# Kernel tuning notes

Measured on AMD Instinct MI355X. Metric: run time of the kernel, lower is better.

Reference implementation:

```python
import jax, jax.numpy as jnp
import numpy as np

C = 16      # internal_channel
G = 8       # deform groups
KK = 9      # 3x3 kernel taps


def conv2d(x, w, b, pad):
    y = jax.lax.conv_general_dilated(
        x, w, window_strides=(1, 1), padding=[(pad, pad), (pad, pad)],
        dimension_numbers=('NCHW', 'OIHW', 'NCHW'))
    return y + b[None, :, None, None]


def feature_extraction(img, p):
    f1 = jax.nn.relu(conv2d(img, p['conv1_w'], p['conv1_b'], 1))   # [B,C,H,W]
    f2 = jax.nn.relu(conv2d(f1, p['conv2_w'], p['conv2_b'], 0))    # [B,C,H-2,W-2]
    f3 = jax.nn.relu(conv2d(f2, p['conv3_w'], p['conv3_b'], 0))    # [B,C,H-4,W-4]
    return [f1, f2, f3]


def deform_conv2d(x, offset, w, b, groups):
    # torchvision deform_conv2d semantics: stride 1, pad 1, dilation 1, 3x3,
    # zero out-of-bounds bilinear sampling, explicit offsets.
    B, Ci, H, W = x.shape
    Cg = Ci // groups
    off = offset.reshape(B, groups, KK, 2, H, W)
    oy, ox = off[:, :, :, 0], off[:, :, :, 1]          # [B,G,K,H,W]
    k = jnp.arange(KK)
    ky = (k // 3).reshape(1, 1, KK, 1, 1).astype(x.dtype)
    kx = (k % 3).reshape(1, 1, KK, 1, 1).astype(x.dtype)
    hh = jnp.arange(H, dtype=x.dtype).reshape(1, 1, 1, H, 1)
    ww = jnp.arange(W, dtype=x.dtype).reshape(1, 1, 1, 1, W)
    ys = hh - 1.0 + ky + oy                            # sample rows
    xs = ww - 1.0 + kx + ox                            # sample cols
    y0 = jnp.floor(ys); x0 = jnp.floor(xs)
    dy = ys - y0; dx = xs - x0
    y0i = y0.astype(jnp.int32); x0i = x0.astype(jnp.int32)
    xg = x.reshape(B, groups, Cg, H * W)

    def gather(iy, ix):
        valid = ((iy >= 0) & (iy < H) & (ix >= 0) & (ix < W)).astype(x.dtype)
        idx = jnp.clip(iy, 0, H - 1) * W + jnp.clip(ix, 0, W - 1)
        g = jnp.take_along_axis(xg, idx.reshape(B, groups, 1, KK * H * W), axis=3)
        return g.reshape(B, groups, Cg, KK, H, W) * valid[:, :, None]

    v = (gather(y0i, x0i) * ((1 - dy) * (1 - dx))[:, :, None]
         + gather(y0i, x0i + 1) * ((1 - dy) * dx)[:, :, None]
         + gather(y0i + 1, x0i) * (dy * (1 - dx))[:, :, None]
         + gather(y0i + 1, x0i + 1) * (dy * dx)[:, :, None])
    v = v.reshape(B, Ci, KK, H, W)
    out = jnp.einsum('ocK,bcKhw->bohw', w.reshape(w.shape[0], Ci, KK), v)
    return out + b[None, :, None, None]


def setup_inputs() -> dict:
    key = jax.random.key(0)
    ks = jax.random.split(key, 12)
    B, H, Wd = 4, 256, 256
    d = {
        'ref_image': jax.random.normal(ks[0], (B, 3, H, Wd), jnp.float32),
        'unreg_image': jax.random.normal(ks[1], (B, 3, H, Wd), jnp.float32),
        'conv1_w': jax.random.normal(ks[2], (C, 3, 3, 3), jnp.float32) * 0.05,
        'conv1_b': jnp.zeros((C,), jnp.float32),
        'conv2_w': jax.random.normal(ks[3], (C, C, 3, 3), jnp.float32) * 0.05,
        'conv2_b': jnp.zeros((C,), jnp.float32),
        'conv3_w': jax.random.normal(ks[4], (C, C, 3, 3), jnp.float32) * 0.05,
        'conv3_b': jnp.zeros((C,), jnp.float32),
        'off1_w': jax.random.normal(ks[5], (2 * G * KK, 2 * C, 3, 3), jnp.float32) * 0.01,
        'off1_b': jnp.zeros((2 * G * KK,), jnp.float32),
        'off2_w': jax.random.normal(ks[6], (2 * G * KK, 2 * C, 3, 3), jnp.float32) * 0.01,
        'off2_b': jnp.zeros((2 * G * KK,), jnp.float32),
        'off3_w': jax.random.normal(ks[7], (2 * G * KK, 2 * C, 3, 3), jnp.float32) * 0.01,
        'off3_b': jnp.zeros((2 * G * KK,), jnp.float32),
        'dcn_w': jax.random.normal(ks[8], (C, C, 3, 3), jnp.float32) * 0.05,
        'dcn_b': jnp.zeros((C,), jnp.float32),
    }
    return d


def reference(ref_image, unreg_image, conv1_w, conv1_b, conv2_w, conv2_b,
              conv3_w, conv3_b, off1_w, off1_b, off2_w, off2_b,
              off3_w, off3_b, dcn_w, dcn_b):
    p = dict(conv1_w=conv1_w, conv1_b=conv1_b, conv2_w=conv2_w, conv2_b=conv2_b,
             conv3_w=conv3_w, conv3_b=conv3_b)
    ref_f = feature_extraction(ref_image, p)
    unr_f = feature_extraction(unreg_image, p)
    off_ws = [(off1_w, off1_b), (off2_w, off2_b), (off3_w, off3_b)]
    aligned = []
    for i in range(3):
        cat = jnp.concatenate([ref_f[i], unr_f[i]], axis=1)          # [B,2C,Hi,Wi]
        offset = jax.nn.relu(conv2d(cat, off_ws[i][0], off_ws[i][1], 1))
        aligned.append(deform_conv2d(unr_f[i], offset, dcn_w, dcn_b, G))
    return tuple(aligned)
```

## Files before the change

kernel.cpp:

```cpp
#include <hip/hip_runtime.h>


typedef __attribute__((ext_vector_type(8))) short bf16x8;
typedef __attribute__((ext_vector_type(4))) float f32x4;
typedef __attribute__((ext_vector_type(2))) float f32x2;

__device__ inline unsigned short f2bf(float f) {
    union { float f; unsigned int u; } x; x.f = f;
    unsigned int u = x.u;
    u += 0x7fffu + ((u >> 16) & 1u);
    return (unsigned short)(u >> 16);
}
__device__ inline float bf2f(unsigned short u) {
    union { unsigned int i; float f; } x; x.i = ((unsigned int)u) << 16;
    return x.f;
}
__device__ inline f32x2 ld2(const float* p) {
    f32x2 v;
    __builtin_memcpy(&v, p, 8);
    return v;
}

__device__ inline void xcd_swz(int& bx, int& by, int& bz) {
    const int gx = gridDim.x, gy = gridDim.y, gz = gridDim.z;
    const int hw = blockIdx.x + gx * (blockIdx.y + gy * blockIdx.z);
    const int per = (gx * gy * gz) >> 3;
    const int lg = (hw & 7) * per + (hw >> 3);
    bz = lg / (gx * gy);
    const int rem = lg - bz * gx * gy;
    by = rem / gx;
    bx = rem - by * gx;
}

__global__ __launch_bounds__(256) void conv1_kernel(
    const float* __restrict__ ref, const float* __restrict__ unr,
    const float* __restrict__ w, const float* __restrict__ bias,
    unsigned short* __restrict__ outA, unsigned short* __restrict__ outB,
    float* __restrict__ pU)
{
    const int H = 256, W = 256;
    __shared__ float sIn[3][18][18];
    const int tx = threadIdx.x, ty = threadIdx.y;
    const int tid = ty * 16 + tx;
    const int bx = blockIdx.x, by = blockIdx.y, bz8 = blockIdx.z;
    const int isUnr = bz8 >> 2, bb = bz8 & 3;
    const float* in = isUnr ? unr : ref;
    unsigned short* outCL = isUnr ? outB : outA;
    const int x0 = bx * 16 - 1, y0 = by * 16 - 1;

    for (int idx = tid; idx < 3 * 324; idx += 256) {
        int c = idx / 324, rem = idx % 324, r = rem / 18, col = rem % 18;
        int gy = y0 + r, gx = x0 + col;
        float v = 0.f;
        if (gy >= 0 && gy < H && gx >= 0 && gx < W)
            v = in[((bb * 3 + c) * H + gy) * W + gx];
        sIn[c][r][col] = v;
    }
    __syncthreads();

    const int y = by * 16 + ty, x = bx * 16 + tx;
    float acc[16];
#pragma unroll
    for (int o = 0; o < 16; o++) acc[o] = bias[o];
#pragma unroll
    for (int ci = 0; ci < 3; ci++) {
        float xv[9];
#pragma unroll
        for (int r = 0; r < 3; r++)
#pragma unroll
            for (int c = 0; c < 3; c++)
                xv[r * 3 + c] = sIn[ci][ty + r][tx + c];
#pragma unroll
        for (int o = 0; o < 16; o++) {
            const float* wp = w + (o * 3 + ci) * 9;
#pragma unroll
            for (int u = 0; u < 9; u++) acc[o] += wp[u] * xv[u];
        }
    }
#pragma unroll
    for (int o = 0; o < 16; o++) acc[o] = fmaxf(acc[o], 0.f);

    const size_t HW = (size_t)H * W;
    unsigned short tmp[16];
#pragma unroll
    for (int o = 0; o < 16; o++) tmp[o] = f2bf(acc[o]);
    unsigned short* op = outCL + ((size_t)bb * HW + (size_t)y * W + x) * 16;
    *(bf16x8*)(op) = *(bf16x8*)&tmp[0];
    *(bf16x8*)(op + 8) = *(bf16x8*)&tmp[8];
    if (isUnr) {
#pragma unroll
        for (int o = 0; o < 16; o++)
            pU[((size_t)(bb * 16 + o) * H + y) * W + x] = acc[o];
    }
}

__global__ __launch_bounds__(512, 4) void c16m_kernel(
    const unsigned short* __restrict__ inA, const unsigned short* __restrict__ inB,
    const unsigned short* __restrict__ Bc16, const float* __restrict__ bias,
    unsigned short* __restrict__ outA, unsigned short* __restrict__ outB,
    float* __restrict__ pU, int Hout, int Wout)
{
    const int Hin = Hout + 2, Win = Wout + 2;
    __shared__ __align__(16) unsigned short sC[324 * 16];
    __shared__ float sT[16][16][17];
    const int tid = threadIdx.x;
    const int bx = blockIdx.x, by = blockIdx.y, bz8 = blockIdx.z;
    const int isUnr = bz8 >> 2, bz = bz8 & 3;
    const unsigned short* inCL = isUnr ? inB : inA;
    unsigned short* outCL = isUnr ? outB : outA;
    const int x0 = bx * 16, y0 = by * 16;

    for (int idx = tid; idx < 648; idx += 512) {
        int px = idx >> 1, half = idx & 1;
        int r = px / 18, c = px % 18;
        int gy = min(y0 + r, Hin - 1), gx = min(x0 + c, Win - 1);
        const bf16x8* p = (const bf16x8*)(inCL +
            (((size_t)bz * Hin * Win + (size_t)gy * Win + gx) * 16 + 8 * half));
        *(bf16x8*)&sC[px * 16 + 8 * half] = *p;
    }
    __syncthreads();

    const int w = tid >> 6, l = tid & 63;
    const int q = l >> 4, j16 = l & 15;
    const float bv = bias[j16];
    f32x4 acc0 = {bv, bv, bv, bv}, acc1 = {bv, bv, bv, bv};

#pragma unroll
    for (int t = 0; t < 5; ++t) {
        const int u = (t == 4) ? 8 : 2 * t + (q >> 1);
        const int dr = u / 3, dc = u % 3;
        bf16x8 a0 = *(const bf16x8*)&sC[(((w) + dr) * 18 + (j16 + dc)) * 16 + (q & 1) * 8];
        bf16x8 a1 = *(const bf16x8*)&sC[(((w + 8) + dr) * 18 + (j16 + dc)) * 16 + (q & 1) * 8];
        bf16x8 b = *(const bf16x8*)&Bc16[(t * 64 + l) * 8];
        acc0 = __builtin_amdgcn_mfma_f32_16x16x32_bf16(a0, b, acc0, 0, 0, 0);
        acc1 = __builtin_amdgcn_mfma_f32_16x16x32_bf16(a1, b, acc1, 0, 0, 0);
    }
#pragma unroll
    for (int r = 0; r < 4; ++r) { acc0[r] = fmaxf(acc0[r], 0.f); acc1[r] = fmaxf(acc1[r], 0.f); }

    const int yA = y0 + w, yB = y0 + w + 8;
    const size_t HWo = (size_t)Hout * Wout;
#pragma unroll
    for (int r = 0; r < 4; ++r) {
        int x = x0 + 4 * q + r;
        if (yA < Hout && x < Wout)
            outCL[((size_t)bz * HWo + (size_t)yA * Wout + x) * 16 + j16] = f2bf(acc0[r]);
        if (yB < Hout && x < Wout)
            outCL[((size_t)bz * HWo + (size_t)yB * Wout + x) * 16 + j16] = f2bf(acc1[r]);
    }

    if (isUnr) {
#pragma unroll
        for (int r = 0; r < 4; ++r) {
            sT[w][j16][4 * q + r] = acc0[r];
            sT[w + 8][j16][4 * q + r] = acc1[r];
        }
        __syncthreads();
        const int ch = tid >> 5, yy = (tid >> 1) & 15, half = tid & 1;
        const int yo = y0 + yy;
        if (yo < Hout) {
            float* dst = pU + ((size_t)(bz * 16 + ch) * Hout + yo) * Wout + x0 + half * 8;
#pragma unroll
            for (int i = 0; i < 8; ++i) {
                int x = x0 + half * 8 + i;
                if (x < Wout) dst[i] = sT[yy][ch][half * 8 + i];
            }
        }
    }
}

__global__ __launch_bounds__(512) void prep_kernel(
    const float* __restrict__ o1w, const float* __restrict__ o2w, const float* __restrict__ o3w,
    const float* __restrict__ o1b, const float* __restrict__ o2b, const float* __restrict__ o3b,
    const float* __restrict__ dw, const float* __restrict__ c2w, const float* __restrict__ c3w,
    unsigned short* __restrict__ Bfrag, float* __restrict__ biasPrep, float* __restrict__ dwT,
    unsigned short* __restrict__ Bc16)
{
    const int lvl = blockIdx.y;
    const float* Wt = (lvl == 0) ? o1w : (lvl == 1) ? o2w : o3w;
    const float* Bb = (lvl == 0) ? o1b : (lvl == 1) ? o2b : o3b;
    int idx = blockIdx.x * 512 + threadIdx.x;
    int j = idx & 7;
    int l = (idx >> 3) & 63;
    int tu = idx >> 9;
    int t = tu / 9, u = tu % 9;
    int q = l >> 4, n16 = l & 15;
    int ci = 8 * q + j;
    int g = n16 >> 1, d = n16 & 1;
    int ch = g * 18 + t * 2 + d;
    Bfrag[lvl * 41472 + idx] = f2bf(Wt[(ch * 32 + ci) * 9 + u]);
    if (blockIdx.x == 0 && threadIdx.x < 144) {
        int n = threadIdx.x;
        int tt = n >> 4, nn = n & 15;
        biasPrep[lvl * 144 + n] = Bb[(nn >> 1) * 18 + tt * 2 + (nn & 1)];
    }
    if (lvl == 0 && blockIdx.x == 1) {
        for (int i = threadIdx.x; i < 2304; i += 512) {
            int c = i / 144, rem = i % 144, k = rem / 16, o = rem & 15;
            dwT[i] = dw[(o * 16 + c) * 9 + k];
        }
    }
    if (lvl == 2 && blockIdx.x >= 20 && blockIdx.x < 30) {
        int i2 = (blockIdx.x - 20) * 512 + threadIdx.x;
        int cw = i2 / 2560, rem = i2 % 2560;
        int jj = rem & 7, ll = (rem >> 3) & 63, tt = rem >> 9;
        int qq = ll >> 4, oo = ll & 15;
        int uu = (tt == 4) ? 8 : 2 * tt + (qq >> 1);
        int cc = (qq & 1) * 8 + jj;
        const float* wsel = cw ? c3w : c2w;
        float val = (tt == 4 && qq >= 2) ? 0.f : wsel[(oo * 16 + cc) * 9 + uu];
        Bc16[i2] = f2bf(val);
    }
}

#define CP 40
__global__ __launch_bounds__(512, 4) void offconv_kernel(
    const unsigned short* __restrict__ refCL, const unsigned short* __restrict__ unrCL,
    const unsigned short* __restrict__ Bfrag, const float* __restrict__ biasPrep,
    unsigned short* __restrict__ offbuf, int bbBase, int BN, int H, int W)
{
    __shared__ __align__(16) unsigned short sIn[18 * 18 * CP];
    __shared__ __align__(16) unsigned short sB[2][4608];
    const int tid = threadIdx.x;
    int bx, by, bz;
    xcd_swz(bx, by, bz);
    const int bb = bbBase + bz;
    const int x0 = bx * 16 - 1, y0 = by * 16 - 1;
    const size_t HW = (size_t)H * W;

    auto loadB = [&](int t, int buf) {
        const bf16x8* src = (const bf16x8*)(Bfrag + (size_t)t * 4608);
        bf16x8* dst = (bf16x8*)&sB[buf][0];
        dst[tid] = src[tid];
        if (tid < 64) dst[512 + tid] = src[512 + tid];
    };
    loadB(0, 0);

    for (int idx = tid; idx < 1296; idx += 512) {
        int px = idx >> 2, ch8 = idx & 3;
        int r = px / 18, c = px % 18;
        int gy = y0 + r, gx = x0 + c;
        bf16x8 v = {};
        if (gy >= 0 && gy < H && gx >= 0 && gx < W) {
            const unsigned short* src = (ch8 < 2) ? refCL : unrCL;
            v = *(const bf16x8*)(src + (((size_t)bb * HW + (size_t)gy * W + gx) * 16 + (ch8 & 1) * 8));
        }
        *(bf16x8*)&sIn[px * CP + ch8 * 8] = v;
    }
    __syncthreads();

    const int w = tid >> 6, l = tid & 63;
    const int q = l >> 4, j16 = l & 15;

    bf16x8 a0[9], a1[9];
#pragma unroll
    for (int u = 0; u < 9; ++u) {
        int dr = u / 3, dc = u % 3;
        a0[u] = *(const bf16x8*)&sIn[((w + dr) * 18 + (j16 + dc)) * CP + 8 * q];
        a1[u] = *(const bf16x8*)&sIn[((w + 8 + dr) * 18 + (j16 + dc)) * CP + 8 * q];
    }
    const int yA = by * 16 + w, yB = by * 16 + w + 8;

    float bvv[9];
#pragma unroll
    for (int t = 0; t < 9; ++t) bvv[t] = biasPrep[t * 16 + j16];

#pragma unroll 1
    for (int t = 0; t < 9; ++t) {
        if (t < 8) loadB(t + 1, (t + 1) & 1);
        const unsigned short* bp = &sB[t & 1][0];
        const float bv = bvv[t];
        f32x4 acc0 = {bv, bv, bv, bv}, acc1 = {bv, bv, bv, bv};
#pragma unroll
        for (int u = 0; u < 9; ++u) {
            bf16x8 b = *(const bf16x8*)&bp[(u * 64 + l) * 8];
            acc0 = __builtin_amdgcn_mfma_f32_16x16x32_bf16(a0[u], b, acc0, 0, 0, 0);
            acc1 = __builtin_amdgcn_mfma_f32_16x16x32_bf16(a1[u], b, acc1, 0, 0, 0);
        }
        const size_t tb = ((size_t)t * BN + bz) * HW;
#pragma unroll
        for (int r = 0; r < 4; ++r) {
            int x = bx * 16 + 4 * q + r;
            if (yA < H && x < W)
                offbuf[(tb + (size_t)yA * W + x) * 16 + j16] = f2bf(fmaxf(acc0[r], 0.f));
            if (yB < H && x < W)
                offbuf[(tb + (size_t)yB * W + x) * 16 + j16] = f2bf(fmaxf(acc1[r], 0.f));
        }
        __syncthreads();
    }
}

__global__ __launch_bounds__(256) void deform_kernel(
    const float* __restrict__ unrP, const unsigned short* __restrict__ offbuf,
    const float* __restrict__ dwT, const float* __restrict__ dcn_b,
    float* __restrict__ out, int bbBase, int BN, int H, int W)
{
    const int tx = threadIdx.x & 15, ty = threadIdx.x >> 4;
    int bxs, bys, bz;
    xcd_swz(bxs, bys, bz);
    const int bb = bbBase + bz;
    const int xr = bxs * 16 + tx, yr = bys * 16 + ty;
    const int x = min(xr, W - 1), y = min(yr, H - 1);
    const size_t HW = (size_t)H * W;
    const float* base = unrP + (size_t)bb * 16 * HW;
    const size_t pxi = (size_t)y * W + x;

    f32x4 pv[4];
#pragma unroll
    for (int i = 0; i < 4; ++i)
        pv[i] = (f32x4){dcn_b[4 * i], dcn_b[4 * i + 1], dcn_b[4 * i + 2], dcn_b[4 * i + 3]};

#pragma unroll 1
    for (int k = 0; k < 9; ++k) {
        const unsigned short* po = offbuf + (((size_t)k * BN + bz) * HW + pxi) * 16;
        bf16x8 s0 = *(const bf16x8*)(po);
        bf16x8 s1 = *(const bf16x8*)(po + 8);
        float ov[16];
#pragma unroll
        for (int i = 0; i < 8; ++i) ov[i] = bf2f((unsigned short)s0[i]);
#pragma unroll
        for (int i = 0; i < 8; ++i) ov[8 + i] = bf2f((unsigned short)s1[i]);

        const float fy = (float)(y - 1 + k / 3);
        const float fx = (float)(x - 1 + k % 3);
#pragma unroll
        for (int g = 0; g < 8; ++g) {
            float oy = ov[2 * g], ox = ov[2 * g + 1];
            float ys = fy + oy, xs = fx + ox;
            float y0f = floorf(ys), x0f = floorf(xs);
            float dy = ys - y0f, dx = xs - x0f;
            int iy0 = (int)y0f, ix0 = (int)x0f;
            int iy1 = iy0 + 1, ix1 = ix0 + 1;
            float vy0 = (iy0 >= 0 && iy0 < H) ? 1.f : 0.f;
            float vy1 = (iy1 >= 0 && iy1 < H) ? 1.f : 0.f;
            float vx0 = (ix0 >= 0 && ix0 < W) ? 1.f : 0.f;
            float vx1 = (ix1 < W) ? 1.f : 0.f;
            int pb = min(max(ix0, 0), W - 2);
            const bool swp = (ix0 != pb);
            float wx0 = (1.f - dx) * vx0, wx1 = dx * vx1;
            float wA = swp ? wx1 : wx0;
            float wB = swp ? wx0 : wx1;
            float wy0 = (1.f - dy) * vy0, wy1 = dy * vy1;
            int cy0 = min(max(iy0, 0), H - 1), cy1 = min(max(iy1, 0), H - 1);
            const float* p0 = base + (size_t)(2 * g) * HW;
            const float* p1 = base + (size_t)(2 * g + 1) * HW;
            const int ib0 = cy0 * W + pb, ib1 = cy1 * W + pb;
            f32x2 a0 = ld2(p0 + ib0), a1 = ld2(p0 + ib1);
            f32x2 b0 = ld2(p1 + ib0), b1 = ld2(p1 + ib1);
            float wA0 = wy0 * wA, wB0 = wy0 * wB, wA1 = wy1 * wA, wB1 = wy1 * wB;
            float v0 = wA0 * a0.x + wB0 * a0.y + wA1 * a1.x + wB1 * a1.y;
            float v1 = wA0 * b0.x + wB0 * b0.y + wA1 * b1.x + wB1 * b1.y;
            const f32x4* wv0 = (const f32x4*)(dwT + ((2 * g) * 9 + k) * 16);
            const f32x4* wv1 = (const f32x4*)(dwT + ((2 * g + 1) * 9 + k) * 16);
#pragma unroll
            for (int i = 0; i < 4; ++i) pv[i] += v0 * wv0[i];
#pragma unroll
            for (int i = 0; i < 4; ++i) pv[i] += v1 * wv1[i];
        }
    }

    if (xr < W && yr < H) {
#pragma unroll
        for (int i = 0; i < 4; ++i)
#pragma unroll
            for (int c = 0; c < 4; ++c)
                out[((size_t)(bb * 16 + 4 * i + c) * H + y) * W + x] = pv[i][c];
    }
}

extern "C" void kernel_launch(void* const* d_in, const int* in_sizes, int n_in,
                              void* d_out, int out_size, void* d_ws, size_t ws_size,
                              hipStream_t stream) {
    (void)in_sizes; (void)n_in; (void)out_size;
    const float* ref = (const float*)d_in[0];
    const float* unr = (const float*)d_in[1];
    const float* c1w = (const float*)d_in[2];  const float* c1b = (const float*)d_in[3];
    const float* c2w = (const float*)d_in[4];  const float* c2b = (const float*)d_in[5];
    const float* c3w = (const float*)d_in[6];  const float* c3b = (const float*)d_in[7];
    const float* o1w = (const float*)d_in[8];  const float* o1b = (const float*)d_in[9];
    const float* o2w = (const float*)d_in[10]; const float* o2b = (const float*)d_in[11];
    const float* o3w = (const float*)d_in[12]; const float* o3b = (const float*)d_in[13];
    const float* dw  = (const float*)d_in[14]; const float* db  = (const float*)d_in[15];

    float* out0 = (float*)d_out;
    float* out1 = out0 + (size_t)4 * 16 * 256 * 256;
    float* out2 = out1 + (size_t)4 * 16 * 254 * 254;

    unsigned short* fA = (unsigned short*)d_ws;
    unsigned short* fB = fA + (size_t)4 * 65536 * 16;
    unsigned short* fC = fB + (size_t)4 * 65536 * 16;
    unsigned short* fD = fC + (size_t)4 * 64516 * 16;
    float* pU = (float*)(fD + (size_t)4 * 64516 * 16);
    unsigned short* BfragBase = (unsigned short*)(pU + (size_t)4 * 16 * 65536);
    unsigned short* Bc16 = BfragBase + 3 * 41472;
    float* biasPrep = (float*)(Bc16 + 2 * 2560);
    float* dwT = biasPrep + 3 * 144;
    unsigned short* offbuf = (unsigned short*)(dwT + 2304);

    const size_t used = (size_t)((char*)offbuf - (char*)d_ws);
    const size_t slice1 = (size_t)256 * 256 * 144;
    const int NB = (ws_size >= used + 4 * slice1 * 2) ? 4 : 1;

    dim3 blk(16, 16);
    prep_kernel<<<dim3(81, 3), 512, 0, stream>>>(o1w, o2w, o3w, o1b, o2b, o3b,
                                                 dw, c2w, c3w,
                                                 BfragBase, biasPrep, dwT, Bc16);
    conv1_kernel<<<dim3(16, 16, 8), blk, 0, stream>>>(ref, unr, c1w, c1b, fA, fB, pU);

    for (int lvl = 0; lvl < 3; ++lvl) {
        const unsigned short *rf, *uf; float* o; int H;
        const unsigned short* Bf = BfragBase + lvl * 41472;
        const float* bp = biasPrep + lvl * 144;
        if (lvl == 0) { rf = fA; uf = fB; o = out0; H = 256; }
        else if (lvl == 1) { rf = fC; uf = fD; o = out1; H = 254; }
        else { rf = fA; uf = fB; o = out2; H = 252; }

        if (NB == 4) {
            offconv_kernel<<<dim3(16, 16, 4), 512, 0, stream>>>(rf, uf, Bf, bp, offbuf, 0, 4, H, H);
            deform_kernel<<<dim3(16, 16, 4), 256, 0, stream>>>(pU, offbuf, dwT, db, o, 0, 4, H, H);
        } else {
            for (int b = 0; b < 4; ++b) {
                offconv_kernel<<<dim3(16, 16, 1), 512, 0, stream>>>(rf, uf, Bf, bp, offbuf, b, 1, H, H);
                deform_kernel<<<dim3(16, 16, 1), 256, 0, stream>>>(pU, offbuf, dwT, db, o, b, 1, H, H);
            }
        }

        if (lvl == 0) {
            c16m_kernel<<<dim3(16, 16, 8), 512, 0, stream>>>(fA, fB, Bc16, c2b, fC, fD, pU, 254, 254);
        } else if (lvl == 1) {
            c16m_kernel<<<dim3(16, 16, 8), 512, 0, stream>>>(fC, fD, Bc16 + 2560, c3b, fA, fB, pU, 252, 252);
        }
    }
}
```

Baseline: 352.0 us.

## Move deform conv channel mixing onto bf16 MFMA via LDS-staged samples

The deform kernel used to accumulate each sampled value into 16 output channels with scalar FMAs against fp32 weights. It now writes the bilinear samples as packed bf16 into shared memory, two taps at a time, and reduces over channels×taps with 16x16x32 bf16 MFMA instructions against a pre-packed weight fragment built in prep_kernel. Results go through LDS so they can be stored per pixel. This removes the per-pixel FMA work but adds bf16 rounding of the samples and weights, LDS traffic, and two barriers per chunk.

Result: faster. 307.6 us, median of 2 (-12.6%).

```diff
diff --git a/kernel.cpp b/kernel.cpp
--- a/kernel.cpp
+++ b/kernel.cpp
@@ -173,8 +173,8 @@
     const float* __restrict__ o1w, const float* __restrict__ o2w, const float* __restrict__ o3w,
     const float* __restrict__ o1b, const float* __restrict__ o2b, const float* __restrict__ o3b,
     const float* __restrict__ dw, const float* __restrict__ c2w, const float* __restrict__ c3w,
-    unsigned short* __restrict__ Bfrag, float* __restrict__ biasPrep, float* __restrict__ dwT,
-    unsigned short* __restrict__ Bc16)
+    unsigned short* __restrict__ Bfrag, float* __restrict__ biasPrep,
+    unsigned short* __restrict__ Bc16, unsigned short* __restrict__ dwB)
 {
     const int lvl = blockIdx.y;
     const float* Wt = (lvl == 0) ? o1w : (lvl == 1) ? o2w : o3w;
@@ -195,9 +195,14 @@
         biasPrep[lvl * 144 + n] = Bb[(nn >> 1) * 18 + tt * 2 + (nn & 1)];
     }
     if (lvl == 0 && blockIdx.x == 1) {
-        for (int i = threadIdx.x; i < 2304; i += 512) {
-            int c = i / 144, rem = i % 144, k = rem / 16, o = rem & 15;
-            dwT[i] = dw[(o * 16 + c) * 9 + k];
+        for (int i = threadIdx.x; i < 2560; i += 512) {
+            int jj = i & 7, l2 = (i >> 3) & 63, chn = i >> 9;
+            int q2 = l2 >> 4, o = l2 & 15;
+            int kkl = 8 * q2 + jj;
+            int gg = kkl >> 2, tl = (kkl >> 1) & 1, dd = kkl & 1;
+            int tt = 2 * chn + tl, cc = 2 * gg + dd;
+            float val = (tt < 9) ? dw[(o * 16 + cc) * 9 + tt] : 0.f;
+            dwB[i] = f2bf(val);
         }
     }
     if (lvl == 2 && blockIdx.x >= 20 && blockIdx.x < 30) {
@@ -292,10 +297,12 @@
 
 __global__ __launch_bounds__(256) void deform_kernel(
     const float* __restrict__ unrP, const unsigned short* __restrict__ offbuf,
-    const float* __restrict__ dwT, const float* __restrict__ dcn_b,
+    const unsigned short* __restrict__ dwB, const float* __restrict__ dcn_b,
     float* __restrict__ out, int bbBase, int BN, int H, int W)
 {
-    const int tx = threadIdx.x & 15, ty = threadIdx.x >> 4;
+    __shared__ __align__(16) unsigned int sA[256 * 20];
+    const int tid = threadIdx.x;
+    const int tx = tid & 15, ty = tid >> 4;
     int bxs, bys, bz;
     xcd_swz(bxs, bys, bz);
     const int bb = bbBase + bz;
@@ -305,66 +312,96 @@
     const float* base = unrP + (size_t)bb * 16 * HW;
     const size_t pxi = (size_t)y * W + x;
 
-    f32x4 pv[4];
-#pragma unroll
-    for (int i = 0; i < 4; ++i)
-        pv[i] = (f32x4){dcn_b[4 * i], dcn_b[4 * i + 1], dcn_b[4 * i + 2], dcn_b[4 * i + 3]};
+    const int wv = tid >> 6, l = tid & 63, q = l >> 4, j16 = l & 15;
+    const float bvb = dcn_b[j16];
+    f32x4 acc0 = {bvb, bvb, bvb, bvb}, acc1 = acc0, acc2 = acc0, acc3 = acc0;
 
 #pragma unroll 1
-    for (int k = 0; k < 9; ++k) {
-        const unsigned short* po = offbuf + (((size_t)k * BN + bz) * HW + pxi) * 16;
-        bf16x8 s0 = *(const bf16x8*)(po);
-        bf16x8 s1 = *(const bf16x8*)(po + 8);
-        float ov[16];
-#pragma unroll
-        for (int i = 0; i < 8; ++i) ov[i] = bf2f((unsigned short)s0[i]);
-#pragma unroll
-        for (int i = 0; i < 8; ++i) ov[8 + i] = bf2f((unsigned short)s1[i]);
-
-        const float fy = (float)(y - 1 + k / 3);
-        const float fx = (float)(x - 1 + k % 3);
-#pragma unroll
-        for (int g = 0; g < 8; ++g) {
-            float oy = ov[2 * g], ox = ov[2 * g + 1];
-            float ys = fy + oy, xs = fx + ox;
-            float y0f = floorf(ys), x0f = floorf(xs);
-            float dy = ys - y0f, dx = xs - x0f;
-            int iy0 = (int)y0f, ix0 = (int)x0f;
-            int iy1 = iy0 + 1, ix1 = ix0 + 1;
-            float vy0 = (iy0 >= 0 && iy0 < H) ? 1.f : 0.f;
-            float vy1 = (iy1 >= 0 && iy1 < H) ? 1.f : 0.f;
-            float vx0 = (ix0 >= 0 && ix0 < W) ? 1.f : 0.f;
-            float vx1 = (ix1 < W) ? 1.f : 0.f;
-            int pb = min(max(ix0, 0), W - 2);
-            const bool swp = (ix0 != pb);
-            float wx0 = (1.f - dx) * vx0, wx1 = dx * vx1;
-            float wA = swp ? wx1 : wx0;
-            float wB = swp ? wx0 : wx1;
-            float wy0 = (1.f - dy) * vy0, wy1 = dy * vy1;
-            int cy0 = min(max(iy0, 0), H - 1), cy1 = min(max(iy1, 0), H - 1);
-            const float* p0 = base + (size_t)(2 * g) * HW;
-            const float* p1 = base + (size_t)(2 * g + 1) * HW;
-            const int ib0 = cy0 * W + pb, ib1 = cy1 * W + pb;
-            f32x2 a0 = ld2(p0 + ib0), a1 = ld2(p0 + ib1);
-            f32x2 b0 = ld2(p1 + ib0), b1 = ld2(p1 + ib1);
-            float wA0 = wy0 * wA, wB0 = wy0 * wB, wA1 = wy1 * wA, wB1 = wy1 * wB;
-            float v0 = wA0 * a0.x + wB0 * a0.y + wA1 * a1.x + wB1 * a1.y;
-            float v1 = wA0 * b0.x + wB0 * b0.y + wA1 * b1.x + wB1 * b1.y;
-            const f32x4* wv0 = (const f32x4*)(dwT + ((2 * g) * 9 + k) * 16);
-            const f32x4* wv1 = (const f32x4*)(dwT + ((2 * g + 1) * 9 + k) * 16);
-#pragma unroll
-            for (int i = 0; i < 4; ++i) pv[i] += v0 * wv0[i];
-#pragma unroll
-            for (int i = 0; i < 4; ++i) pv[i] += v1 * wv1[i];
-        }
-    }
+    for (int chn = 0; chn < 5; ++chn) {
+#pragma unroll
+        for (int tl = 0; tl < 2; ++tl) {
+            const int t = 2 * chn + tl;
+            if (t < 9) {
+                const unsigned short* po = offbuf + (((size_t)t * BN + bz) * HW + pxi) * 16;
+                bf16x8 s0 = *(const bf16x8*)(po);
+                bf16x8 s1 = *(const bf16x8*)(po + 8);
+                float ov[16];
+#pragma unroll
+                for (int i = 0; i < 8; ++i) ov[i] = bf2f((unsigned short)s0[i]);
+#pragma unroll
+                for (int i = 0; i < 8; ++i) ov[8 + i] = bf2f((unsigned short)s1[i]);
+
+                const float fy = (float)(y - 1 + t / 3);
+                const float fx = (float)(x - 1 + t % 3);
+#pragma unroll
+                for (int g = 0; g < 8; ++g) {
+                    float oy = ov[2 * g], ox = ov[2 * g + 1];
+                    float ys = fy + oy, xs = fx + ox;
+                    float y0f = floorf(ys), x0f = floorf(xs);
+                    float dy = ys - y0f, dx = xs - x0f;
+                    int iy0 = (int)y0f, ix0 = (int)x0f;
+                    int iy1 = iy0 + 1, ix1 = ix0 + 1;
+                    float vy0 = (iy0 >= 0 && iy0 < H) ? 1.f : 0.f;
+                    float vy1 = (iy1 >= 0 && iy1 < H) ? 1.f : 0.f;
+                    float vx0 = (ix0 >= 0 && ix0 < W) ? 1.f : 0.f;
+                    float vx1 = (ix1 < W) ? 1.f : 0.f;
+                    int pb = min(max(ix0, 0), W - 2);
+                    const bool swp = (ix0 != pb);
+                    float wx0 = (1.f - dx) * vx0, wx1 = dx * vx1;
+                    float wA = swp ? wx1 : wx0;
+                    float wB = swp ? wx0 : wx1;
+                    float wy0 = (1.f - dy) * vy0, wy1 = dy * vy1;
+                    int cy0 = min(max(iy0, 0), H - 1), cy1 = min(max(iy1, 0), H - 1);
+                    const float* p0 = base + (size_t)(2 * g) * HW;
+                    const float* p1 = base + (size_t)(2 * g + 1) * HW;
+                    const int ib0 = cy0 * W + pb, ib1 = cy1 * W + pb;
+                    f32x2 a0 = ld2(p0 + ib0), a1 = ld2(p0 + ib1);
+                    f32x2 b0 = ld2(p1 + ib0), b1 = ld2(p1 + ib1);
+                    float wA0 = wy0 * wA, wB0 = wy0 * wB, wA1 = wy1 * wA, wB1 = wy1 * wB;
+                    float v0 = wA0 * a0.x + wB0 * a0.y + wA1 * a1.x + wB1 * a1.y;
+                    float v1 = wA0 * b0.x + wB0 * b0.y + wA1 * b1.x + wB1 * b1.y;
+                    sA[tid * 20 + g * 2 + tl] =
+                        (unsigned int)f2bf(v0) | ((unsigned int)f2bf(v1) << 16);
+                }
+            } else {
+#pragma unroll
+                for (int g = 0; g < 8; ++g) sA[tid * 20 + g * 2 + tl] = 0u;
+            }
+        }
+        __syncthreads();
+        bf16x8 b = *(const bf16x8*)((const unsigned short*)dwB + (size_t)(chn * 64 + l) * 8);
+        {
+            bf16x8 a;
+            a = *(const bf16x8*)&sA[((4 * wv + 0) * 16 + j16) * 20 + 4 * q];
+            acc0 = __builtin_amdgcn_mfma_f32_16x16x32_bf16(a, b, acc0, 0, 0, 0);
+            a = *(const bf16x8*)&sA[((4 * wv + 1) * 16 + j16) * 20 + 4 * q];
+            acc1 = __builtin_amdgcn_mfma_f32_16x16x32_bf16(a, b, acc1, 0, 0, 0);
+            a = *(const bf16x8*)&sA[((4 * wv + 2) * 16 + j16) * 20 + 4 * q];
+            acc2 = __builtin_amdgcn_mfma_f32_16x16x32_bf16(a, b, acc2, 0, 0, 0);
+            a = *(const bf16x8*)&sA[((4 * wv + 3) * 16 + j16) * 20 + 4 * q];
+            acc3 = __builtin_amdgcn_mfma_f32_16x16x32_bf16(a, b, acc3, 0, 0, 0);
+        }
+        __syncthreads();
+    }
+
+    unsigned int* sT = sA;
+#pragma unroll
+    for (int r = 0; r < 4; ++r) {
+        union { float f; unsigned int u; } cvt;
+        cvt.f = acc0[r]; sT[((4 * wv + 0) * 16 + 4 * q + r) * 17 + j16] = cvt.u;
+        cvt.f = acc1[r]; sT[((4 * wv + 1) * 16 + 4 * q + r) * 17 + j16] = cvt.u;
+        cvt.f = acc2[r]; sT[((4 * wv + 2) * 16 + 4 * q + r) * 17 + j16] = cvt.u;
+        cvt.f = acc3[r]; sT[((4 * wv + 3) * 16 + 4 * q + r) * 17 + j16] = cvt.u;
+    }
+    __syncthreads();
 
     if (xr < W && yr < H) {
 #pragma unroll
-        for (int i = 0; i < 4; ++i)
-#pragma unroll
-            for (int c = 0; c < 4; ++c)
-                out[((size_t)(bb * 16 + 4 * i + c) * H + y) * W + x] = pv[i][c];
+        for (int o = 0; o < 16; ++o) {
+            union { unsigned int u; float f; } cvt;
+            cvt.u = sT[tid * 17 + o];
+            out[((size_t)(bb * 16 + o) * H + y) * W + x] = cvt.f;
+        }
     }
 }
 
@@ -393,9 +430,9 @@
     float* pU = (float*)(fD + (size_t)4 * 64516 * 16);
     unsigned short* BfragBase = (unsigned short*)(pU + (size_t)4 * 16 * 65536);
     unsigned short* Bc16 = BfragBase + 3 * 41472;
-    float* biasPrep = (float*)(Bc16 + 2 * 2560);
-    float* dwT = biasPrep + 3 * 144;
-    unsigned short* offbuf = (unsigned short*)(dwT + 2304);
+    unsigned short* dwB = Bc16 + 2 * 2560;
+    float* biasPrep = (float*)(dwB + 2560);
+    unsigned short* offbuf = (unsigned short*)(biasPrep + 3 * 144);
 
     const size_t used = (size_t)((char*)offbuf - (char*)d_ws);
     const size_t slice1 = (size_t)256 * 256 * 144;
@@ -404,7 +441,7 @@
     dim3 blk(16, 16);
     prep_kernel<<<dim3(81, 3), 512, 0, stream>>>(o1w, o2w, o3w, o1b, o2b, o3b,
                                                  dw, c2w, c3w,
-                                                 BfragBase, biasPrep, dwT, Bc16);
+                                                 BfragBase, biasPrep, Bc16, dwB);
     conv1_kernel<<<dim3(16, 16, 8), blk, 0, stream>>>(ref, unr, c1w, c1b, fA, fB, pU);
 
     for (int lvl = 0; lvl < 3; ++lvl) {
@@ -417,11 +454,11 @@
 
         if (NB == 4) {
             offconv_kernel<<<dim3(16, 16, 4), 512, 0, stream>>>(rf, uf, Bf, bp, offbuf, 0, 4, H, H);
-            deform_kernel<<<dim3(16, 16, 4), 256, 0, stream>>>(pU, offbuf, dwT, db, o, 0, 4, H, H);
+            deform_kernel<<<dim3(16, 16, 4), 256, 0, stream>>>(pU, offbuf, dwB, db, o, 0, 4, H, H);
         } else {
             for (int b = 0; b < 4; ++b) {
                 offconv_kernel<<<dim3(16, 16, 1), 512, 0, stream>>>(rf, uf, Bf, bp, offbuf, b, 1, H, H);
-                deform_kernel<<<dim3(16, 16, 1), 256, 0, stream>>>(pU, offbuf, dwT, db, o, b, 1, H, H);
+                deform_kernel<<<dim3(16, 16, 1), 256, 0, stream>>>(pU, offbuf, dwB, db, o, b, 1, H, H);
             }
         }
 
```
